# Performance work log

Measured on AMD Instinct MI355X. Metric: run time of the kernel, lower is better.

Reference implementation:

```python
import jax, jax.numpy as jnp
import numpy as np

MASK_FILL = float(-2**32 + 1)


def setup_inputs() -> dict:
    key = jax.random.key(0)
    k1, k2, k3, k4, k5 = jax.random.split(key, 5)
    B, T, D = 64, 1024, 128
    return {
        "key": jax.random.normal(k1, (B, T, D), dtype=jnp.float32),
        "value": jax.random.normal(k2, (B, T, D), dtype=jnp.float32),
        "query": jax.random.normal(k3, (B, T, D), dtype=jnp.float32),
        "mask": jax.random.randint(k4, (B, T, T), 0, 2).astype(jnp.bool_),
        "query_mask": jax.random.uniform(k5, (B, T, 1), dtype=jnp.float32),
        "num_hidden": D,
    }


def reference(key, value, query, mask, query_mask, num_hidden):
    # scores: [B, Tq, Tk]
    scale = 1.0 / jnp.sqrt(jnp.float32(num_hidden))
    attn = jnp.einsum("bqd,bkd->bqk", query, key) * scale
    attn = jnp.where(mask, MASK_FILL, attn)
    attn = jax.nn.softmax(attn, axis=-1)
    attn = attn * query_mask  # broadcast [B, Tq, 1]
    result = jnp.einsum("bqk,bkd->bqd", attn, value)
    return (result, attn)
```

## Files before the change

### kernel.cpp

```cpp
#include <hip/hip_runtime.h>

#define B_   64
#define T_   1024
#define D_   128
#define SCALE_ 0.08838834764831845f
#define FILL_  (-4294967295.0f)
#define VST  132

typedef __attribute__((ext_vector_type(8))) short short8v;
typedef __attribute__((ext_vector_type(4))) float f32x4;

#define MFMA16(A,Bv,C) __builtin_amdgcn_mfma_f32_16x16x32_bf16((A),(Bv),(C),0,0,0)

__device__ __forceinline__ void split8(const float f[8], short8v& h, short8v& l) {
#pragma unroll
    for (int i = 0; i < 8; ++i) {
        const unsigned int u = __float_as_uint(f[i]);
        h[i] = (short)(u >> 16);
        const float r = f[i] - __uint_as_float(u & 0xffff0000u);
        l[i] = (short)(__float_as_uint(r) >> 16);
    }
}
__device__ __forceinline__ unsigned int packsplit(float f) {
    const unsigned int u = __float_as_uint(f);
    const unsigned int hi = u >> 16;
    const float r = f - __uint_as_float(u & 0xffff0000u);
    const unsigned int lo = __float_as_uint(r) >> 16;
    return hi | (lo << 16);
}

__global__ __launch_bounds__(512, 4)
void mha_kernel(const float* __restrict__ Kp, const float* __restrict__ Vp,
                const float* __restrict__ Qp, const unsigned char* __restrict__ Mp,
                const float* __restrict__ QMp, float* __restrict__ Orp,
                float* __restrict__ Oap)
{
    __shared__ __align__(16) float Vlds[64 * VST];
    __shared__ unsigned int Pc[64 * 33];
    __shared__ float redA[8 * 32];
    __shared__ float redB[8 * 32];

    const int tid  = threadIdx.x;
    const int w    = tid >> 6;
    const int lane = tid & 63;
    const int g    = lane >> 4;
    const int c    = lane & 15;
    const int wg   = (blockIdx.x & 7) * 256 + (blockIdx.x >> 3);
    const int b    = wg >> 5;
    const int q0   = (wg & 31) << 5;

    const unsigned int* mw = (const unsigned int*)Mp;
    unsigned int bad = 0u;
#pragma unroll
    for (int i = 0; i < 16; ++i) bad |= (unsigned int)(mw[i] > 1u);
    const bool m32 = (bad == 0u);

    const size_t bt = (size_t)b * T_;

    f32x4 acc[2][8];
#pragma unroll
    for (int mt = 0; mt < 2; ++mt)
#pragma unroll
        for (int nt = 0; nt < 8; ++nt) acc[mt][nt] = (f32x4)0.f;

#pragma unroll
    for (int ks = 0; ks < 4; ++ks) {
        short8v qh[2], ql[2];
#pragma unroll
        for (int mt = 0; mt < 2; ++mt) {
            const float* qp = Qp + (bt + q0 + mt*16 + c) * D_ + ks*32 + g*8;
            float f[8];
#pragma unroll
            for (int i = 0; i < 8; ++i) f[i] = qp[i];
            split8(f, qh[mt], ql[mt]);
        }
#pragma unroll
        for (int nt = 0; nt < 8; ++nt) {
            const float* kp = Kp + (bt + w*128 + nt*16 + c) * D_ + ks*32 + g*8;
            float f[8];
#pragma unroll
            for (int i = 0; i < 8; ++i) f[i] = kp[i];
            short8v kh, kl;
            split8(f, kh, kl);
#pragma unroll
            for (int mt = 0; mt < 2; ++mt) {
                acc[mt][nt] = MFMA16(qh[mt], kh, acc[mt][nt]);
                acc[mt][nt] = MFMA16(qh[mt], kl, acc[mt][nt]);
                acc[mt][nt] = MFMA16(ql[mt], kh, acc[mt][nt]);
            }
        }
    }

    float rmax[2][4];
#pragma unroll
    for (int mt = 0; mt < 2; ++mt)
#pragma unroll
    for (int rg = 0; rg < 4; ++rg) {
        const int row = mt*16 + g*4 + rg;
        const size_t mrow = (bt + q0 + row) * (size_t)T_ + w*128;
        float rm = -3.0e38f;
        if (m32) {
            const int* mi = (const int*)Mp;
#pragma unroll
            for (int nt = 0; nt < 8; ++nt) {
                float s = acc[mt][nt][rg] * SCALE_;
                if (mi[mrow + nt*16 + c]) s = FILL_;
                acc[mt][nt][rg] = s;
                rm = fmaxf(rm, s);
            }
        } else {
#pragma unroll
            for (int nt = 0; nt < 8; ++nt) {
                float s = acc[mt][nt][rg] * SCALE_;
                if (Mp[mrow + nt*16 + c]) s = FILL_;
                acc[mt][nt][rg] = s;
                rm = fmaxf(rm, s);
            }
        }
        rmax[mt][rg] = rm;
    }
#pragma unroll
    for (int mt = 0; mt < 2; ++mt)
#pragma unroll
    for (int rg = 0; rg < 4; ++rg)
#pragma unroll
        for (int off = 1; off < 16; off <<= 1)
            rmax[mt][rg] = fmaxf(rmax[mt][rg], __shfl_xor(rmax[mt][rg], off, 64));
    if (c == 0) {
#pragma unroll
        for (int mt = 0; mt < 2; ++mt)
#pragma unroll
        for (int rg = 0; rg < 4; ++rg)
            redA[w*32 + mt*16 + g*4 + rg] = rmax[mt][rg];
    }
    __syncthreads();
    float rsum[2][4];
#pragma unroll
    for (int mt = 0; mt < 2; ++mt)
#pragma unroll
    for (int rg = 0; rg < 4; ++rg) {
        const int row = mt*16 + g*4 + rg;
        float m = redA[row];
#pragma unroll
        for (int w2 = 1; w2 < 8; ++w2) m = fmaxf(m, redA[w2*32 + row]);
        float s = 0.f;
#pragma unroll
        for (int nt = 0; nt < 8; ++nt) {
            const float e = __expf(acc[mt][nt][rg] - m);
            acc[mt][nt][rg] = e;
            s += e;
        }
#pragma unroll
        for (int off = 1; off < 16; off <<= 1) s += __shfl_xor(s, off, 64);
        rsum[mt][rg] = s;
    }
    if (c == 0) {
#pragma unroll
        for (int mt = 0; mt < 2; ++mt)
#pragma unroll
        for (int rg = 0; rg < 4; ++rg)
            redB[w*32 + mt*16 + g*4 + rg] = rsum[mt][rg];
    }
    __syncthreads();

    unsigned int pk[2][8][4];
#pragma unroll
    for (int mt = 0; mt < 2; ++mt)
#pragma unroll
    for (int rg = 0; rg < 4; ++rg) {
        const int row = mt*16 + g*4 + rg;
        float ssum = redB[row];
#pragma unroll
        for (int w2 = 1; w2 < 8; ++w2) ssum += redB[w2*32 + row];
        const float inv = QMp[bt + q0 + row] / ssum;
        const size_t arow = (bt + q0 + row) * (size_t)T_ + w*128;
#pragma unroll
        for (int nt = 0; nt < 8; ++nt) {
            const float p = acc[mt][nt][rg] * inv;
            Oap[arow + nt*16 + c] = p;
            pk[mt][nt][rg] = packsplit(p);
        }
    }

    f32x4 o[2];
    o[0] = (f32x4)0.f;
    o[1] = (f32x4)0.f;

    const int vrow = tid >> 3;
    const int vcg  = tid & 7;

#define WRITE_P(NB)                                                        \
    {                                                                      \
        _Pragma("unroll")                                                  \
        for (int mt = 0; mt < 2; ++mt)                                     \
        _Pragma("unroll")                                                  \
        for (int n4 = 0; n4 < 4; ++n4)                                     \
        _Pragma("unroll")                                                  \
        for (int rg = 0; rg < 4; ++rg)                                     \
            Pc[(n4*16 + c)*33 + mt*16 + g*4 + rg] = pk[mt][(NB) + n4][rg]; \
    }

    for (int kc = 0; kc < 16; ++kc) {
        __syncthreads();
        if (w == (kc >> 1)) {
            if (kc & 1) { WRITE_P(4) } else { WRITE_P(0) }
        }
        {
            const float* vp = Vp + (bt + kc*64 + vrow) * D_ + vcg*16;
            float* dst = &Vlds[vrow * VST + ((vcg ^ ((vrow >> 3) & 3)) << 4)];
#pragma unroll
            for (int j = 0; j < 4; ++j)
                *(float4*)&dst[j*4] = *(const float4*)&vp[j*4];
        }
        __syncthreads();
#pragma unroll
        for (int ks2 = 0; ks2 < 2; ++ks2) {
            short8v ph[2], pl[2];
#pragma unroll
            for (int mt = 0; mt < 2; ++mt) {
                const int base = (ks2*32 + g*8)*33 + mt*16 + c;
#pragma unroll
                for (int i = 0; i < 8; ++i) {
                    const unsigned int x = Pc[base + i*33];
                    ph[mt][i] = (short)(x & 0xffffu);
                    pl[mt][i] = (short)(x >> 16);
                }
            }
            float fv[8];
            {
                const int kb   = ks2*32 + g*8;
                const int dsw  = (w*16 + c) ^ ((((kb) >> 3) & 3) << 4);
                const int base = kb * VST + dsw;
#pragma unroll
                for (int i = 0; i < 8; ++i) fv[i] = Vlds[base + i * VST];
            }
            short8v vh, vl;
            split8(fv, vh, vl);
#pragma unroll
            for (int mt = 0; mt < 2; ++mt) {
                o[mt] = MFMA16(ph[mt], vh, o[mt]);
                o[mt] = MFMA16(ph[mt], vl, o[mt]);
                o[mt] = MFMA16(pl[mt], vh, o[mt]);
            }
        }
    }

#pragma unroll
    for (int mt = 0; mt < 2; ++mt)
#pragma unroll
    for (int rg = 0; rg < 4; ++rg)
        Orp[(bt + q0 + mt*16 + g*4 + rg) * D_ + w*16 + c] = o[mt][rg];
}

extern "C" void kernel_launch(void* const* d_in, const int* in_sizes, int n_in,
                              void* d_out, int out_size, void* d_ws, size_t ws_size,
                              hipStream_t stream)
{
    const float* Kp  = (const float*)d_in[0];
    const float* Vp  = (const float*)d_in[1];
    const float* Qp  = (const float*)d_in[2];
    const unsigned char* Mp = (const unsigned char*)d_in[3];
    const float* QMp = (const float*)d_in[4];
    float* Orp = (float*)d_out;
    float* Oap = Orp + (size_t)B_ * T_ * D_;

    hipLaunchKernelGGL(mha_kernel, dim3(B_ * 32), dim3(512), 0, stream,
                       Kp, Vp, Qp, Mp, QMp, Orp, Oap);
}
```

Before: 861.4 us.

## Read V directly from global memory, widen P chunks, use nontemporal stores

```diff
diff --git a/kernel.cpp b/kernel.cpp
--- a/kernel.cpp
+++ b/kernel.cpp
@@ -5,7 +5,6 @@
 #define D_   128
 #define SCALE_ 0.08838834764831845f
 #define FILL_  (-4294967295.0f)
-#define VST  132
 
 typedef __attribute__((ext_vector_type(8))) short short8v;
 typedef __attribute__((ext_vector_type(4))) float f32x4;
@@ -35,8 +34,7 @@
                 const float* __restrict__ QMp, float* __restrict__ Orp,
                 float* __restrict__ Oap)
 {
-    __shared__ __align__(16) float Vlds[64 * VST];
-    __shared__ unsigned int Pc[64 * 33];
+    __shared__ unsigned int Pc[128 * 33];
     __shared__ float redA[8 * 32];
     __shared__ float redB[8 * 32];
 
@@ -177,7 +175,7 @@
 #pragma unroll
         for (int nt = 0; nt < 8; ++nt) {
             const float p = acc[mt][nt][rg] * inv;
-            Oap[arow + nt*16 + c] = p;
+            __builtin_nontemporal_store(p, &Oap[arow + nt*16 + c]);
             pk[mt][nt][rg] = packsplit(p);
         }
     }
@@ -186,35 +184,20 @@
     o[0] = (f32x4)0.f;
     o[1] = (f32x4)0.f;
 
-    const int vrow = tid >> 3;
-    const int vcg  = tid & 7;
-
-#define WRITE_P(NB)                                                        \
-    {                                                                      \
-        _Pragma("unroll")                                                  \
-        for (int mt = 0; mt < 2; ++mt)                                     \
-        _Pragma("unroll")                                                  \
-        for (int n4 = 0; n4 < 4; ++n4)                                     \
-        _Pragma("unroll")                                                  \
-        for (int rg = 0; rg < 4; ++rg)                                     \
-            Pc[(n4*16 + c)*33 + mt*16 + g*4 + rg] = pk[mt][(NB) + n4][rg]; \
-    }
-
-    for (int kc = 0; kc < 16; ++kc) {
+    for (int kc = 0; kc < 8; ++kc) {
         __syncthreads();
-        if (w == (kc >> 1)) {
-            if (kc & 1) { WRITE_P(4) } else { WRITE_P(0) }
-        }
-        {
-            const float* vp = Vp + (bt + kc*64 + vrow) * D_ + vcg*16;
-            float* dst = &Vlds[vrow * VST + ((vcg ^ ((vrow >> 3) & 3)) << 4)];
-#pragma unroll
-            for (int j = 0; j < 4; ++j)
-                *(float4*)&dst[j*4] = *(const float4*)&vp[j*4];
+        if (w == kc) {
+#pragma unroll
+            for (int mt = 0; mt < 2; ++mt)
+#pragma unroll
+            for (int nt = 0; nt < 8; ++nt)
+#pragma unroll
+            for (int rg = 0; rg < 4; ++rg)
+                Pc[(nt*16 + c)*33 + mt*16 + g*4 + rg] = pk[mt][nt][rg];
         }
         __syncthreads();
 #pragma unroll
-        for (int ks2 = 0; ks2 < 2; ++ks2) {
+        for (int ks2 = 0; ks2 < 4; ++ks2) {
             short8v ph[2], pl[2];
 #pragma unroll
             for (int mt = 0; mt < 2; ++mt) {
@@ -228,11 +211,9 @@
             }
             float fv[8];
             {
-                const int kb   = ks2*32 + g*8;
-                const int dsw  = (w*16 + c) ^ ((((kb) >> 3) & 3) << 4);
-                const int base = kb * VST + dsw;
-#pragma unroll
-                for (int i = 0; i < 8; ++i) fv[i] = Vlds[base + i * VST];
+                const float* vp = Vp + (bt + kc*128 + ks2*32 + g*8) * D_ + w*16 + c;
+#pragma unroll
+                for (int i = 0; i < 8; ++i) fv[i] = vp[(size_t)i * D_];
             }
             short8v vh, vl;
             split8(fv, vh, vl);
@@ -249,7 +230,8 @@
     for (int mt = 0; mt < 2; ++mt)
 #pragma unroll
     for (int rg = 0; rg < 4; ++rg)
-        Orp[(bt + q0 + mt*16 + g*4 + rg) * D_ + w*16 + c] = o[mt][rg];
+        __builtin_nontemporal_store(o[mt][rg],
+            &Orp[(bt + q0 + mt*16 + g*4 + rg) * D_ + w*16 + c]);
 }
 
 extern "C" void kernel_launch(void* const* d_in, const int* in_sizes, int n_in,
```

New measurement: 829.3 us. 3.7% less time.
